# Kernel tuning notes

Hardware: AMD Instinct MI355X
Metric: run time of the kernel (lower is better)

The kernel has to match this reference:

```python
import jax, jax.numpy as jnp
import numpy as np

B, N, D, H = 2, 2048, 512, 8
HD = D // H


def setup_inputs() -> dict:
    key = jax.random.key(0)
    ks = jax.random.split(key, 12)
    s = 1.0 / np.sqrt(D)
    inp = {
        "x": jax.random.normal(ks[0], (B, N, D), dtype=jnp.float32),
        "adjacency": jax.random.randint(ks[1], (B, N, N), 0, 2, dtype=jnp.int32),
        "Wq": jax.random.uniform(ks[2], (D, D), jnp.float32, -s, s),
        "bq": jnp.zeros((D,), jnp.float32),
        "Wk": jax.random.uniform(ks[3], (D, D), jnp.float32, -s, s),
        "bk": jnp.zeros((D,), jnp.float32),
        "Wv": jax.random.uniform(ks[4], (D, D), jnp.float32, -s, s),
        "bv": jnp.zeros((D,), jnp.float32),
        "Wo": jax.random.uniform(ks[5], (D, D), jnp.float32, -s, s),
        "bo": jnp.zeros((D,), jnp.float32),
        "gamma": jnp.ones((D,), jnp.float32),
        "beta": jnp.zeros((D,), jnp.float32),
    }
    return inp


def reference(x, adjacency, Wq, bq, Wk, bk, Wv, bv, Wo, bo, gamma, beta):
    scale = HD ** -0.5
    # projections -> [B, H, N, HD]
    def proj(W, b):
        return (x @ W.T + b).reshape(B, N, H, HD).transpose(0, 2, 1, 3)
    q = proj(Wq, bq)
    k = proj(Wk, bk)
    v = proj(Wv, bv)
    # [B, H, N, N] attention scores
    scores = jnp.einsum("bhqd,bhkd->bhqk", q, k) * scale
    mask = (adjacency[:, None, :, :] != 0)  # [B, 1->H, N, N]
    scores = jnp.where(mask, scores, -jnp.inf)
    attn = jax.nn.softmax(scores, axis=-1)
    # dropout is identity in eval mode
    ctx = jnp.einsum("bhqk,bhkd->bhqd", attn, v)
    ctx = ctx.transpose(0, 2, 1, 3).reshape(B, N, D)
    out = ctx @ Wo.T + bo
    y = x + out
    mu = jnp.mean(y, axis=-1, keepdims=True)
    var = jnp.var(y, axis=-1, keepdims=True)
    return (y - mu) * jax.lax.rsqrt(var + 1e-5) * gamma + beta
```

## Files before the change

kernel.cpp:

```cpp
#include <hip/hip_runtime.h>
#include <hip/hip_bf16.h>

#define B_  2
#define N_  2048
#define D_  512
#define H_  8
#define HD_ 64

typedef float  f4  __attribute__((ext_vector_type(4)));
typedef int    i4  __attribute__((ext_vector_type(4)));
typedef short  bf16x8 __attribute__((ext_vector_type(8)));
typedef float  f32x4  __attribute__((ext_vector_type(4)));
typedef unsigned short u16x8 __attribute__((ext_vector_type(8)));

static __device__ __forceinline__ unsigned short f2bf(float f) {
    union { float f; unsigned int u; } v; v.f = f;
    unsigned int r = v.u + 0x7fffu + ((v.u >> 16) & 1u);
    return (unsigned short)(r >> 16);
}

__global__ __launch_bounds__(256) void prep_kernel(
    const float* __restrict__ x,
    const float* __restrict__ Wq, const float* __restrict__ Wk,
    const float* __restrict__ Wv, const float* __restrict__ Wo,
    unsigned short* __restrict__ xh, unsigned short* __restrict__ WhAll)
{
    const size_t e = ((size_t)blockIdx.x * 256 + threadIdx.x) * 8;
    const float* src;
    unsigned short* dst;
    if (e < 2097152) {
        src = x + e;  dst = xh + e;
    } else {
        const size_t e2 = e - 2097152;
        const int wi = (int)(e2 >> 18);
        const size_t off = e2 & 262143;
        const float* Ws = (wi == 0) ? Wq : (wi == 1) ? Wk : (wi == 2) ? Wv : Wo;
        src = Ws + off;  dst = WhAll + (size_t)wi * 262144 + off;
    }
    f4 a = *(const f4*)src;
    f4 b = *(const f4*)(src + 4);
    u16x8 o;
    #pragma unroll
    for (int j = 0; j < 4; ++j) { o[j] = f2bf(a[j]); o[j + 4] = f2bf(b[j]); }
    *(u16x8*)dst = o;
}

template <int OUT_MODE>
__device__ __forceinline__ void mfma_gemm_body(
    const unsigned short* __restrict__ Ah, const unsigned short* __restrict__ Wh,
    const float* __restrict__ bias, float* __restrict__ outf,
    unsigned short* __restrict__ outh, int r0, int c0)
{
    __shared__ unsigned short Asm[128][72];
    __shared__ unsigned short Bsm[128][72];

    const int tid  = threadIdx.x;
    const int lane = tid & 63;
    const int w    = tid >> 6;
    const int wr   = w >> 1, wc = w & 1;
    const int l15  = lane & 15, lhi = lane >> 4;

    f32x4 acc[4][4];
    #pragma unroll
    for (int mi = 0; mi < 4; ++mi)
        #pragma unroll
        for (int ni = 0; ni < 4; ++ni)
            acc[mi][ni] = (f32x4){0.f, 0.f, 0.f, 0.f};

    for (int kt = 0; kt < 512; kt += 64) {
        __syncthreads();
        #pragma unroll
        for (int i = 0; i < 4; ++i) {
            const int v   = tid + i * 256;
            const int row = v >> 3;
            const int c8  = (v & 7) * 8;
            *(u16x8*)&Asm[row][c8] =
                *(const u16x8*)&Ah[(size_t)(r0 + row) * 512 + kt + c8];
            *(u16x8*)&Bsm[row][c8] =
                *(const u16x8*)&Wh[(size_t)(c0 + row) * 512 + kt + c8];
        }
        __syncthreads();

        #pragma unroll
        for (int ks = 0; ks < 2; ++ks) {
            bf16x8 a[4], bb[4];
            #pragma unroll
            for (int mi = 0; mi < 4; ++mi)
                a[mi] = *(const bf16x8*)&Asm[wr * 64 + mi * 16 + l15][ks * 32 + lhi * 8];
            #pragma unroll
            for (int ni = 0; ni < 4; ++ni)
                bb[ni] = *(const bf16x8*)&Bsm[wc * 64 + ni * 16 + l15][ks * 32 + lhi * 8];
            #pragma unroll
            for (int mi = 0; mi < 4; ++mi)
                #pragma unroll
                for (int ni = 0; ni < 4; ++ni)
                    acc[mi][ni] = __builtin_amdgcn_mfma_f32_16x16x32_bf16(
                        a[mi], bb[ni], acc[mi][ni], 0, 0, 0);
        }
    }

    #pragma unroll
    for (int ni = 0; ni < 4; ++ni) {
        const int c = c0 + wc * 64 + ni * 16 + l15;
        const float bias_c = bias[c];
        #pragma unroll
        for (int mi = 0; mi < 4; ++mi) {
            #pragma unroll
            for (int reg = 0; reg < 4; ++reg) {
                const int r = r0 + wr * 64 + mi * 16 + lhi * 4 + reg;
                const float vv = acc[mi][ni][reg] + bias_c;
                if (OUT_MODE == 0) {
                    outf[(size_t)r * 512 + c] = vv;
                } else {
                    const int bbn = r >> 11, n = r & (N_ - 1);
                    const int h = c >> 6, hd = c & 63;
                    outh[(((size_t)(bbn * H_ + h)) * N_ + n) * HD_ + hd] = f2bf(vv);
                }
            }
        }
    }
}

__global__ __launch_bounds__(256) void qkv_mfma_kernel(
    const unsigned short* __restrict__ xh, const unsigned short* __restrict__ WhAll,
    const float* __restrict__ bq, const float* __restrict__ bk,
    const float* __restrict__ bv,
    unsigned short* __restrict__ Qh, unsigned short* __restrict__ Kh,
    unsigned short* __restrict__ Vh)
{
    const int z = blockIdx.z;
    const unsigned short* Wh = WhAll + (size_t)z * 262144;
    const float* bias = (z == 0) ? bq : (z == 1) ? bk : bv;
    unsigned short* dst = (z == 0) ? Qh : (z == 1) ? Kh : Vh;
    mfma_gemm_body<1>(xh, Wh, bias, nullptr, dst,
                      blockIdx.y * 128, blockIdx.x * 128);
}

__global__ __launch_bounds__(256) void wo_mfma_kernel(
    const unsigned short* __restrict__ ctxh, const unsigned short* __restrict__ WhAll,
    const float* __restrict__ bo, float* __restrict__ y1)
{
    mfma_gemm_body<0>(ctxh, WhAll + 3 * 262144, bo, y1, nullptr,
                      blockIdx.y * 128, blockIdx.x * 128);
}

__global__ __launch_bounds__(256) void attn_kernel(
    const unsigned short* __restrict__ Q, const unsigned short* __restrict__ K,
    const unsigned short* __restrict__ V, const int* __restrict__ adj,
    unsigned short* __restrict__ ctxh)
{
    __shared__ unsigned short K_lds[64][72];
    __shared__ unsigned short Vt_lds[64][72];
    __shared__ unsigned short P_lds[4][16][72];

    const int tid  = threadIdx.x;
    const int lane = tid & 63;
    const int w    = tid >> 6;
    const int l15  = lane & 15, lhi = lane >> 4;
    const int bh = blockIdx.y;
    const int b  = bh >> 3;
    const int hh = bh & 7;
    const int q0 = blockIdx.x * 64;

    const unsigned short* Qbh = Q + (size_t)bh * N_ * HD_;
    const unsigned short* Kbh = K + (size_t)bh * N_ * HD_;
    const unsigned short* Vbh = V + (size_t)bh * N_ * HD_;
    const int* adjb = adj + (size_t)b * N_ * N_;

    const int qrow = q0 + w * 16 + l15;
    bf16x8 aq0 = *(const bf16x8*)&Qbh[(size_t)qrow * HD_ + lhi * 8];
    bf16x8 aq1 = *(const bf16x8*)&Qbh[(size_t)qrow * HD_ + 32 + lhi * 8];

    const int qrow_base = q0 + w * 16 + lhi * 4;

    f32x4 acc[4];
    #pragma unroll
    for (int t = 0; t < 4; ++t) acc[t] = (f32x4){0.f, 0.f, 0.f, 0.f};
    float m_r[4], l_r[4];
    const float NEG_INF = -__builtin_inff();
    #pragma unroll
    for (int r = 0; r < 4; ++r) { m_r[r] = NEG_INF; l_r[r] = 0.0f; }

    const float scale = 0.125f;

    int adjc[4][4], adjn[4][4];
    #pragma unroll
    for (int r = 0; r < 4; ++r)
        #pragma unroll
        for (int kt = 0; kt < 4; ++kt)
            adjc[r][kt] = adjb[(size_t)(qrow_base + r) * N_ + kt * 16 + l15];

    for (int kc = 0; kc < N_; kc += 64) {
        __syncthreads();

        {
            const int k  = tid & 63;
            const int c2 = tid >> 6;
            u16x8 k0 = *(const u16x8*)&Kbh[(size_t)(kc + k) * HD_ + c2 * 8];
            u16x8 k1 = *(const u16x8*)&Kbh[(size_t)(kc + k) * HD_ + (c2 + 4) * 8];
            *(u16x8*)&K_lds[k][c2 * 8]       = k0;
            *(u16x8*)&K_lds[k][(c2 + 4) * 8] = k1;
        }
        {
            const int k2  = (tid & 31) * 2;
            const int dvb = (tid >> 5) * 8;
            u16x8 v0 = *(const u16x8*)&Vbh[(size_t)(kc + k2) * HD_ + dvb];
            u16x8 v1 = *(const u16x8*)&Vbh[(size_t)(kc + k2 + 1) * HD_ + dvb];
            #pragma unroll
            for (int i = 0; i < 8; ++i) {
                unsigned int pair = (unsigned int)(unsigned short)v0[i] |
                                    ((unsigned int)(unsigned short)v1[i] << 16);
                *(unsigned int*)&Vt_lds[dvb + i][k2] = pair;
            }
        }

        const int kcn = (kc + 64) & (N_ - 1);
        #pragma unroll
        for (int r = 0; r < 4; ++r)
            #pragma unroll
            for (int kt = 0; kt < 4; ++kt)
                adjn[r][kt] = adjb[(size_t)(qrow_base + r) * N_ + kcn + kt * 16 + l15];

        __syncthreads();

        f32x4 s[4];
        #pragma unroll
        for (int kt = 0; kt < 4; ++kt) {
            bf16x8 bk0 = *(const bf16x8*)&K_lds[kt * 16 + l15][lhi * 8];
            bf16x8 bk1 = *(const bf16x8*)&K_lds[kt * 16 + l15][32 + lhi * 8];
            f32x4 z = {0.f, 0.f, 0.f, 0.f};
            z = __builtin_amdgcn_mfma_f32_16x16x32_bf16(aq0, bk0, z, 0, 0, 0);
            s[kt] = __builtin_amdgcn_mfma_f32_16x16x32_bf16(aq1, bk1, z, 0, 0, 0);
        }

        #pragma unroll
        for (int r = 0; r < 4; ++r) {
            float sm[4];
            #pragma unroll
            for (int kt = 0; kt < 4; ++kt)
                sm[kt] = adjc[r][kt] ? s[kt][r] * scale : NEG_INF;
            float mx = fmaxf(fmaxf(sm[0], sm[1]), fmaxf(sm[2], sm[3]));
            #pragma unroll
            for (int off = 1; off < 16; off <<= 1)
                mx = fmaxf(mx, __shfl_xor(mx, off));
            const float mnew = fmaxf(m_r[r], mx);
            float fac, p[4];
            if (mnew == NEG_INF) {
                fac = 1.0f;
                p[0] = p[1] = p[2] = p[3] = 0.0f;
            } else {
                fac = __expf(m_r[r] - mnew);
                #pragma unroll
                for (int kt = 0; kt < 4; ++kt)
                    p[kt] = __expf(sm[kt] - mnew);
            }
            m_r[r] = mnew;
            float rs = p[0] + p[1] + p[2] + p[3];
            #pragma unroll
            for (int off = 1; off < 16; off <<= 1)
                rs += __shfl_xor(rs, off);
            l_r[r] = l_r[r] * fac + rs;
            #pragma unroll
            for (int t = 0; t < 4; ++t) acc[t][r] *= fac;
            #pragma unroll
            for (int kt = 0; kt < 4; ++kt)
                P_lds[w][lhi * 4 + r][kt * 16 + l15] = f2bf(p[kt]);
        }

        #pragma unroll
        for (int ks = 0; ks < 2; ++ks) {
            bf16x8 ap = *(const bf16x8*)&P_lds[w][l15][ks * 32 + lhi * 8];
            #pragma unroll
            for (int dvt = 0; dvt < 4; ++dvt) {
                bf16x8 bv = *(const bf16x8*)&Vt_lds[dvt * 16 + l15][ks * 32 + lhi * 8];
                acc[dvt] = __builtin_amdgcn_mfma_f32_16x16x32_bf16(ap, bv, acc[dvt], 0, 0, 0);
            }
        }

        #pragma unroll
        for (int r = 0; r < 4; ++r)
            #pragma unroll
            for (int kt = 0; kt < 4; ++kt)
                adjc[r][kt] = adjn[r][kt];
    }

    #pragma unroll
    for (int r = 0; r < 4; ++r) {
        const int q = qrow_base + r;
        const float inv = (l_r[r] > 0.0f) ? 1.0f / l_r[r] : 0.0f;
        #pragma unroll
        for (int dvt = 0; dvt < 4; ++dvt)
            ctxh[((size_t)(b * N_ + q)) * D_ + hh * HD_ + dvt * 16 + l15] =
                f2bf(acc[dvt][r] * inv);
    }
}

__global__ __launch_bounds__(64) void ln_kernel(
    const float* __restrict__ x, const float* __restrict__ y1,
    const float* __restrict__ gamma, const float* __restrict__ beta,
    float* __restrict__ out)
{
    const int row = blockIdx.x;
    const int tid = threadIdx.x;
    const size_t base = (size_t)row * 512 + tid * 8;

    f4 v0 = *(const f4*)&x[base]     + *(const f4*)&y1[base];
    f4 v1 = *(const f4*)&x[base + 4] + *(const f4*)&y1[base + 4];

    float s = v0[0] + v0[1] + v0[2] + v0[3] + v1[0] + v1[1] + v1[2] + v1[3];
    #pragma unroll
    for (int off = 1; off < 64; off <<= 1) s += __shfl_xor(s, off);
    const float mu = s * (1.0f / 512.0f);

    float d2 = 0.0f;
    #pragma unroll
    for (int j = 0; j < 4; ++j) {
        const float a = v0[j] - mu, bq = v1[j] - mu;
        d2 += a * a + bq * bq;
    }
    #pragma unroll
    for (int off = 1; off < 64; off <<= 1) d2 += __shfl_xor(d2, off);
    const float rstd = rsqrtf(d2 * (1.0f / 512.0f) + 1e-5f);

    f4 g0 = *(const f4*)&gamma[tid * 8];
    f4 g1 = *(const f4*)&gamma[tid * 8 + 4];
    f4 be0 = *(const f4*)&beta[tid * 8];
    f4 be1 = *(const f4*)&beta[tid * 8 + 4];
    f4 o0, o1;
    #pragma unroll
    for (int j = 0; j < 4; ++j) {
        o0[j] = (v0[j] - mu) * rstd * g0[j] + be0[j];
        o1[j] = (v1[j] - mu) * rstd * g1[j] + be1[j];
    }
    *(f4*)&out[base]     = o0;
    *(f4*)&out[base + 4] = o1;
}

extern "C" void kernel_launch(void* const* d_in, const int* in_sizes, int n_in,
                              void* d_out, int out_size, void* d_ws, size_t ws_size,
                              hipStream_t stream)
{
    const float* x     = (const float*)d_in[0];
    const int*   adj   = (const int*)  d_in[1];
    const float* Wq    = (const float*)d_in[2];
    const float* bq    = (const float*)d_in[3];
    const float* Wk    = (const float*)d_in[4];
    const float* bk    = (const float*)d_in[5];
    const float* Wv    = (const float*)d_in[6];
    const float* bv    = (const float*)d_in[7];
    const float* Wo    = (const float*)d_in[8];
    const float* bo    = (const float*)d_in[9];
    const float* gamma = (const float*)d_in[10];
    const float* beta  = (const float*)d_in[11];
    float* out = (float*)d_out;

    const size_t elems = (size_t)B_ * N_ * D_;
    unsigned short* Qh    = (unsigned short*)d_ws;
    unsigned short* Kh    = Qh   + elems;
    unsigned short* Vh    = Kh   + elems;
    unsigned short* ctxh  = Vh   + elems;
    unsigned short* xh    = ctxh + elems;
    unsigned short* WhAll = xh   + elems;
    float* y1 = (float*)Qh;

    prep_kernel<<<1536, 256, 0, stream>>>(x, Wq, Wk, Wv, Wo, xh, WhAll);

    qkv_mfma_kernel<<<dim3(4, 32, 3), 256, 0, stream>>>(
        xh, WhAll, bq, bk, bv, Qh, Kh, Vh);

    attn_kernel<<<dim3(N_ / 64, B_ * H_), 256, 0, stream>>>(Qh, Kh, Vh, adj, ctxh);

    wo_mfma_kernel<<<dim3(4, 32), 256, 0, stream>>>(ctxh, WhAll, bo, y1);

    ln_kernel<<<B_ * N_, 64, 0, stream>>>(x, y1, gamma, beta, out);
}
```

Before: 241.8 us.

## Split attention key range across blocks and merge partial softmax results

Attention is split into two key-range halves via a third grid dimension, each writing unnormalized fp32 partial outputs plus running max and sum. A new combine kernel rescales and merges the two partials and writes the bf16 context. This doubles the block count to improve GPU occupancy and latency hiding, at the cost of extra global traffic for the partials and one additional kernel launch.

```diff
diff --git a/kernel.cpp b/kernel.cpp
--- a/kernel.cpp
+++ b/kernel.cpp
@@ -6,6 +6,8 @@
 #define D_  512
 #define H_  8
 #define HD_ 64
+#define NSPLIT_ 2
+#define KRANGE_ (N_ / NSPLIT_)
 
 typedef float  f4  __attribute__((ext_vector_type(4)));
 typedef int    i4  __attribute__((ext_vector_type(4)));
@@ -144,10 +146,10 @@
                       blockIdx.y * 128, blockIdx.x * 128);
 }
 
-__global__ __launch_bounds__(256) void attn_kernel(
+__global__ __launch_bounds__(256) void attn_split_kernel(
     const unsigned short* __restrict__ Q, const unsigned short* __restrict__ K,
     const unsigned short* __restrict__ V, const int* __restrict__ adj,
-    unsigned short* __restrict__ ctxh)
+    float* __restrict__ Opart, float* __restrict__ ML)
 {
     __shared__ unsigned short K_lds[64][72];
     __shared__ unsigned short Vt_lds[64][72];
@@ -159,8 +161,9 @@
     const int l15  = lane & 15, lhi = lane >> 4;
     const int bh = blockIdx.y;
     const int b  = bh >> 3;
-    const int hh = bh & 7;
     const int q0 = blockIdx.x * 64;
+    const int split = blockIdx.z;
+    const int kbeg  = split * KRANGE_;
 
     const unsigned short* Qbh = Q + (size_t)bh * N_ * HD_;
     const unsigned short* Kbh = K + (size_t)bh * N_ * HD_;
@@ -188,9 +191,9 @@
     for (int r = 0; r < 4; ++r)
         #pragma unroll
         for (int kt = 0; kt < 4; ++kt)
-            adjc[r][kt] = adjb[(size_t)(qrow_base + r) * N_ + kt * 16 + l15];
-
-    for (int kc = 0; kc < N_; kc += 64) {
+            adjc[r][kt] = adjb[(size_t)(qrow_base + r) * N_ + kbeg + kt * 16 + l15];
+
+    for (int kc = kbeg; kc < kbeg + KRANGE_; kc += 64) {
         __syncthreads();
 
         {
@@ -214,7 +217,7 @@
             }
         }
 
-        const int kcn = (kc + 64) & (N_ - 1);
+        const int kcn = kbeg + ((kc - kbeg + 64) & (KRANGE_ - 1));
         #pragma unroll
         for (int r = 0; r < 4; ++r)
             #pragma unroll
@@ -284,15 +287,44 @@
                 adjc[r][kt] = adjn[r][kt];
     }
 
+    float* Osplit = Opart + (size_t)split * (16 * 2048 * 64);
     #pragma unroll
     for (int r = 0; r < 4; ++r) {
         const int q = qrow_base + r;
-        const float inv = (l_r[r] > 0.0f) ? 1.0f / l_r[r] : 0.0f;
         #pragma unroll
         for (int dvt = 0; dvt < 4; ++dvt)
-            ctxh[((size_t)(b * N_ + q)) * D_ + hh * HD_ + dvt * 16 + l15] =
-                f2bf(acc[dvt][r] * inv);
-    }
+            Osplit[((size_t)bh * 2048 + q) * 64 + dvt * 16 + l15] = acc[dvt][r];
+        if (l15 == 0) {
+            float2* ml = (float2*)ML;
+            ml[(size_t)split * 32768 + bh * 2048 + q] =
+                make_float2(m_r[r], l_r[r]);
+        }
+    }
+}
+
+__global__ __launch_bounds__(256) void combine_kernel(
+    const float* __restrict__ Opart, const float* __restrict__ ML,
+    unsigned short* __restrict__ ctxh)
+{
+    const int row  = blockIdx.x * 4 + (threadIdx.x >> 6);
+    const int lane = threadIdx.x & 63;
+    const float NEG_INF = -__builtin_inff();
+
+    const float2 ml0 = ((const float2*)ML)[row];
+    const float2 ml1 = ((const float2*)ML)[32768 + row];
+    const float M  = fmaxf(ml0.x, ml1.x);
+    const float s0 = (ml0.x == NEG_INF) ? 0.0f : __expf(ml0.x - M);
+    const float s1 = (ml1.x == NEG_INF) ? 0.0f : __expf(ml1.x - M);
+    const float L  = ml0.y * s0 + ml1.y * s1;
+    const float inv = (L > 0.0f) ? 1.0f / L : 0.0f;
+
+    const float o0 = Opart[(size_t)row * 64 + lane];
+    const float o1 = Opart[(size_t)(16 * 2048 * 64) + (size_t)row * 64 + lane];
+    const float o  = (o0 * s0 + o1 * s1) * inv;
+
+    const int bh = row >> 11, q = row & 2047;
+    const int b = bh >> 3, hh = bh & 7;
+    ctxh[((size_t)(b * 2048 + q)) * 512 + hh * 64 + lane] = f2bf(o);
 }
 
 __global__ __launch_bounds__(64) void ln_kernel(
@@ -361,6 +393,8 @@
     unsigned short* ctxh  = Vh   + elems;
     unsigned short* xh    = ctxh + elems;
     unsigned short* WhAll = xh   + elems;
+    float* Opart = (float*)(WhAll + 4 * 262144);
+    float* ML    = Opart + 2 * (16 * 2048 * 64);
     float* y1 = (float*)Qh;
 
     prep_kernel<<<1536, 256, 0, stream>>>(x, Wq, Wk, Wv, Wo, xh, WhAll);
@@ -368,7 +402,9 @@
     qkv_mfma_kernel<<<dim3(4, 32, 3), 256, 0, stream>>>(
         xh, WhAll, bq, bk, bv, Qh, Kh, Vh);
 
-    attn_kernel<<<dim3(N_ / 64, B_ * H_), 256, 0, stream>>>(Qh, Kh, Vh, adj, ctxh);
+    attn_split_kernel<<<dim3(N_ / 64, B_ * H_, NSPLIT_), 256, 0, stream>>>(
+        Qh, Kh, Vh, adj, Opart, ML);
+    combine_kernel<<<(16 * 2048) / 4, 256, 0, stream>>>(Opart, ML, ctxh);
 
     wo_mfma_kernel<<<dim3(4, 32), 256, 0, stream>>>(ctxh, WhAll, bo, y1);
 
```

Measured after the change: 243.1 us. No clear change (+0.5%).

## Compute transposed QK^T scores so each lane owns one query row

Applied to the files above, without the earlier changes.

Swaps the MFMA operands so the score tile comes out transposed: each lane holds 16 keys for a single query instead of 4 queries. The row max and sum then mostly reduce inside the lane, with only two cross-lane shuffles instead of four per row, and the adjacency mask is read as contiguous int4 vectors. The per-row rescale factors and final row sums are passed back to the original accumulator layout through a small LDS array, and P is written with 4-wide stores. It relies on intra-wave LDS ordering without a barrier and keeps more scores live in registers.

```diff
diff --git a/kernel.cpp b/kernel.cpp
--- a/kernel.cpp
+++ b/kernel.cpp
@@ -12,6 +12,7 @@
 typedef short  bf16x8 __attribute__((ext_vector_type(8)));
 typedef float  f32x4  __attribute__((ext_vector_type(4)));
 typedef unsigned short u16x8 __attribute__((ext_vector_type(8)));
+typedef unsigned short u16x4 __attribute__((ext_vector_type(4)));
 
 static __device__ __forceinline__ unsigned short f2bf(float f) {
     union { float f; unsigned int u; } v; v.f = f;
@@ -152,6 +153,7 @@
     __shared__ unsigned short K_lds[64][72];
     __shared__ unsigned short Vt_lds[64][72];
     __shared__ unsigned short P_lds[4][16][72];
+    __shared__ float fac_lds[4][16];
 
     const int tid  = threadIdx.x;
     const int lane = tid & 63;
@@ -176,19 +178,15 @@
     f32x4 acc[4];
     #pragma unroll
     for (int t = 0; t < 4; ++t) acc[t] = (f32x4){0.f, 0.f, 0.f, 0.f};
-    float m_r[4], l_r[4];
+    float m_q = -__builtin_inff();
+    float l_q = 0.0f;
     const float NEG_INF = -__builtin_inff();
-    #pragma unroll
-    for (int r = 0; r < 4; ++r) { m_r[r] = NEG_INF; l_r[r] = 0.0f; }
-
     const float scale = 0.125f;
 
-    int adjc[4][4], adjn[4][4];
-    #pragma unroll
-    for (int r = 0; r < 4; ++r)
-        #pragma unroll
-        for (int kt = 0; kt < 4; ++kt)
-            adjc[r][kt] = adjb[(size_t)(qrow_base + r) * N_ + kt * 16 + l15];
+    i4 adjc[4], adjn[4];
+    #pragma unroll
+    for (int kt = 0; kt < 4; ++kt)
+        adjc[kt] = *(const i4*)&adjb[(size_t)qrow * N_ + kt * 16 + lhi * 4];
 
     for (int kc = 0; kc < N_; kc += 64) {
         __syncthreads();
@@ -216,10 +214,8 @@
 
         const int kcn = (kc + 64) & (N_ - 1);
         #pragma unroll
-        for (int r = 0; r < 4; ++r)
-            #pragma unroll
-            for (int kt = 0; kt < 4; ++kt)
-                adjn[r][kt] = adjb[(size_t)(qrow_base + r) * N_ + kcn + kt * 16 + l15];
+        for (int kt = 0; kt < 4; ++kt)
+            adjn[kt] = *(const i4*)&adjb[(size_t)qrow * N_ + kcn + kt * 16 + lhi * 4];
 
         __syncthreads();
 
@@ -229,42 +225,58 @@
             bf16x8 bk0 = *(const bf16x8*)&K_lds[kt * 16 + l15][lhi * 8];
             bf16x8 bk1 = *(const bf16x8*)&K_lds[kt * 16 + l15][32 + lhi * 8];
             f32x4 z = {0.f, 0.f, 0.f, 0.f};
-            z = __builtin_amdgcn_mfma_f32_16x16x32_bf16(aq0, bk0, z, 0, 0, 0);
-            s[kt] = __builtin_amdgcn_mfma_f32_16x16x32_bf16(aq1, bk1, z, 0, 0, 0);
-        }
-
-        #pragma unroll
-        for (int r = 0; r < 4; ++r) {
-            float sm[4];
-            #pragma unroll
-            for (int kt = 0; kt < 4; ++kt)
-                sm[kt] = adjc[r][kt] ? s[kt][r] * scale : NEG_INF;
-            float mx = fmaxf(fmaxf(sm[0], sm[1]), fmaxf(sm[2], sm[3]));
-            #pragma unroll
-            for (int off = 1; off < 16; off <<= 1)
-                mx = fmaxf(mx, __shfl_xor(mx, off));
-            const float mnew = fmaxf(m_r[r], mx);
-            float fac, p[4];
-            if (mnew == NEG_INF) {
-                fac = 1.0f;
-                p[0] = p[1] = p[2] = p[3] = 0.0f;
-            } else {
-                fac = __expf(m_r[r] - mnew);
-                #pragma unroll
-                for (int kt = 0; kt < 4; ++kt)
-                    p[kt] = __expf(sm[kt] - mnew);
-            }
-            m_r[r] = mnew;
-            float rs = p[0] + p[1] + p[2] + p[3];
-            #pragma unroll
-            for (int off = 1; off < 16; off <<= 1)
-                rs += __shfl_xor(rs, off);
-            l_r[r] = l_r[r] * fac + rs;
-            #pragma unroll
-            for (int t = 0; t < 4; ++t) acc[t][r] *= fac;
-            #pragma unroll
-            for (int kt = 0; kt < 4; ++kt)
-                P_lds[w][lhi * 4 + r][kt * 16 + l15] = f2bf(p[kt]);
+            z = __builtin_amdgcn_mfma_f32_16x16x32_bf16(bk0, aq0, z, 0, 0, 0);
+            s[kt] = __builtin_amdgcn_mfma_f32_16x16x32_bf16(bk1, aq1, z, 0, 0, 0);
+        }
+
+        float sm[16];
+        #pragma unroll
+        for (int kt = 0; kt < 4; ++kt)
+            #pragma unroll
+            for (int r = 0; r < 4; ++r)
+                sm[kt * 4 + r] = adjc[kt][r] ? s[kt][r] * scale : NEG_INF;
+
+        float mx = sm[0];
+        #pragma unroll
+        for (int i = 1; i < 16; ++i) mx = fmaxf(mx, sm[i]);
+        mx = fmaxf(mx, __shfl_xor(mx, 16));
+        mx = fmaxf(mx, __shfl_xor(mx, 32));
+
+        const float mnew = fmaxf(m_q, mx);
+        float fac, p[16];
+        if (mnew == NEG_INF) {
+            fac = 1.0f;
+            #pragma unroll
+            for (int i = 0; i < 16; ++i) p[i] = 0.0f;
+        } else {
+            fac = __expf(m_q - mnew);
+            #pragma unroll
+            for (int i = 0; i < 16; ++i)
+                p[i] = __expf(sm[i] - mnew);
+        }
+        m_q = mnew;
+
+        float rs = 0.0f;
+        #pragma unroll
+        for (int i = 0; i < 16; ++i) rs += p[i];
+        rs += __shfl_xor(rs, 16);
+        rs += __shfl_xor(rs, 32);
+        l_q = l_q * fac + rs;
+
+        if (lhi == 0) fac_lds[w][l15] = fac;
+        f4 fac4 = *(const f4*)&fac_lds[w][lhi * 4];
+        #pragma unroll
+        for (int t = 0; t < 4; ++t)
+            #pragma unroll
+            for (int r = 0; r < 4; ++r)
+                acc[t][r] *= fac4[r];
+
+        #pragma unroll
+        for (int kt = 0; kt < 4; ++kt) {
+            u16x4 pw;
+            #pragma unroll
+            for (int r = 0; r < 4; ++r) pw[r] = f2bf(p[kt * 4 + r]);
+            *(u16x4*)&P_lds[w][l15][kt * 16 + lhi * 4] = pw;
         }
 
         #pragma unroll
@@ -278,16 +290,15 @@
         }
 
         #pragma unroll
-        for (int r = 0; r < 4; ++r)
-            #pragma unroll
-            for (int kt = 0; kt < 4; ++kt)
-                adjc[r][kt] = adjn[r][kt];
-    }
-
+        for (int kt = 0; kt < 4; ++kt) adjc[kt] = adjn[kt];
+    }
+
+    if (lhi == 0) fac_lds[w][l15] = l_q;
+    f4 lv = *(const f4*)&fac_lds[w][lhi * 4];
     #pragma unroll
     for (int r = 0; r < 4; ++r) {
         const int q = qrow_base + r;
-        const float inv = (l_r[r] > 0.0f) ? 1.0f / l_r[r] : 0.0f;
+        const float inv = (lv[r] > 0.0f) ? 1.0f / lv[r] : 0.0f;
         #pragma unroll
         for (int dvt = 0; dvt < 4; ++dvt)
             ctxh[((size_t)(b * N_ + q)) * D_ + hh * HD_ + dvt * 16 + l15] =
```

Measured after the change: 225.6 us. -6.7%, faster.
